# Performance work log

Hardware: AMD Instinct MI355X
Metric: run time of the kernel (lower is better)

## Reference

```python
import jax, jax.numpy as jnp
import numpy as np

N_USERS = 100000
N_ITEMS = 50000
N_NODES = N_USERS + N_ITEMS
EMB_DIM = 64
N_EDGES = 4000000
N_LAYERS = 3
BATCH = 4096


def setup_inputs() -> dict:
    key = jax.random.key(0)
    k = jax.random.split(key, 7)
    return {
        "user_emb": jax.random.normal(k[0], (N_USERS, EMB_DIM), dtype=jnp.float32) * 0.1,
        "item_emb": jax.random.normal(k[1], (N_ITEMS, EMB_DIM), dtype=jnp.float32) * 0.1,
        "vals": jax.random.uniform(k[2], (N_EDGES,), dtype=jnp.float32),
        "src": jax.random.randint(k[3], (N_EDGES,), 0, N_NODES, dtype=jnp.int32),
        "dst": jax.random.randint(k[4], (N_EDGES,), 0, N_NODES, dtype=jnp.int32),
        "users": jax.random.randint(k[5], (BATCH,), 0, N_USERS, dtype=jnp.int32),
        "items": jax.random.randint(k[6], (BATCH,), 0, N_ITEMS, dtype=jnp.int32),
    }


def _propagate(user_emb, item_emb, vals, src, dst):
    # all_emb: [N, D]; sparse adjacency A given as COO (src -> dst, weight vals)
    all_emb = jnp.concatenate([user_emb, item_emb], axis=0)
    acc = all_emb  # running sum over layers (layer 0 included)
    emb = all_emb
    for _ in range(N_LAYERS):
        # SpMM: out[d] = sum_{e: dst[e]==d} vals[e] * emb[src[e]]
        msgs = vals[:, None] * emb[src]               # [E, D]
        emb = jax.ops.segment_sum(msgs, dst, num_segments=N_NODES)
        acc = acc + emb
    light_out = acc / jnp.float32(N_LAYERS + 1)       # mean over stacked layers
    return light_out[:N_USERS], light_out[N_USERS:]


def reference(user_emb, item_emb, vals, src, dst, users, items):
    all_users, all_items = _propagate(user_emb, item_emb, vals, src, dst)
    u = all_users[users]                              # [B, D]
    i = all_items[items]                              # [B, D]
    gamma = jnp.sum(u * i, axis=1)                    # [B]
    return gamma
```

## Files before the change

kernel.cpp:

```cpp
#include <hip/hip_runtime.h>
#include <hip/hip_bf16.h>

#define N_USERS 100000
#define N_ITEMS 50000
#define N_NODES 150000
#define DIM 64
#define N_EDGES 4000000
#define BATCH 4096

#define NBKT 256
#define BW 588
#define STRIDE 16640
#define PA_EDGES 4096
#define PA_ITER 16
#define PA_BLOCKS ((N_EDGES + PA_EDGES - 1) / PA_EDGES)
#define CVT_THREADS (N_NODES * DIM / 8)
#define CVT_BLOCKS 512
#define BS_ITER 32

__device__ __forceinline__ float blo(unsigned int u) { return __uint_as_float(u << 16); }
__device__ __forceinline__ float bhi(unsigned int u) { return __uint_as_float(u & 0xffff0000u); }
__device__ __forceinline__ unsigned int f2b(float f) {
    unsigned int x = __float_as_uint(f);
    return (x + 0x7fffu + ((x >> 16) & 1u)) >> 16;
}
__device__ __forceinline__ unsigned int pack2(float a, float b) {
    return f2b(a) | (f2b(b) << 16);
}

typedef float v2f __attribute__((ext_vector_type(2)));

__global__ void __launch_bounds__(256, 4) k_partition(
        const int* __restrict__ src, const int* __restrict__ dst,
        const float* __restrict__ vals,
        int* __restrict__ gcur, int2* __restrict__ tmp) {
    __shared__ int cnt[NBKT];
    __shared__ int base_s[NBKT];
    __shared__ int off_s[NBKT];
    __shared__ int2 rec_s[PA_EDGES];
    __shared__ unsigned char bin_s[PA_EDGES];
    int t = threadIdx.x;
    int myb[PA_ITER];
    int mykey[PA_ITER];
    int myval[PA_ITER];
    size_t base = (size_t)blockIdx.x * PA_EDGES;
#pragma unroll
    for (int it = 0; it < PA_ITER; it++) {
        size_t i = base + (size_t)it * 256 + t;
        if (i < N_EDGES) {
            myb[it] = __builtin_nontemporal_load(dst + i);
            mykey[it] = __builtin_nontemporal_load(src + i);
            myval[it] = __float_as_int(__builtin_nontemporal_load(vals + i));
        } else {
            myb[it] = -1;
        }
    }
    for (int i = t; i < NBKT; i += 256) cnt[i] = 0;
    __syncthreads();
#pragma unroll
    for (int it = 0; it < PA_ITER; it++) {
        int d = myb[it];
        if (d >= 0) {
            int b = d / BW;
            mykey[it] = (mykey[it] << 10) | (d - b * BW);
            myb[it] = b;
            atomicAdd(&cnt[b], 1);
        }
    }
    __syncthreads();
    {
        int bb = (t + blockIdx.x * 37) & (NBKT - 1);
        int c = cnt[bb];
        base_s[bb] = (c > 0) ? atomicAdd(&gcur[bb], c) : 0;
    }
    if (t < 64) {
        int lane = t;
        int carry = 0;
        for (int c = 0; c < NBKT / 64; c++) {
            int i = c * 64 + lane;
            int x = cnt[i];
            int incl = x;
            for (int o = 1; o < 64; o <<= 1) {
                int y = __shfl_up(incl, o);
                if (lane >= o) incl += y;
            }
            off_s[i] = carry + incl - x;
            carry += __shfl(incl, 63);
        }
    }
    __syncthreads();
    for (int i = t; i < NBKT; i += 256) cnt[i] = 0;
    __syncthreads();
#pragma unroll
    for (int it = 0; it < PA_ITER; it++) {
        int b = myb[it];
        if (b >= 0) {
            int pos = off_s[b] + atomicAdd(&cnt[b], 1);
            rec_s[pos] = make_int2(mykey[it], myval[it]);
            bin_s[pos] = (unsigned char)b;
        }
    }
    __syncthreads();
    int nrec = off_s[NBKT - 1] + cnt[NBKT - 1];
    for (int i = t; i < nrec; i += 256) {
        int2 r = rec_s[i];
        int b = bin_s[i];
        tmp[(size_t)b * STRIDE + base_s[b] + (i - off_s[b])] = r;
    }
}

__global__ void k_bsortcvt(const int2* __restrict__ tmp, const int* __restrict__ gcur,
                           int* __restrict__ row_ptr, int2* __restrict__ fin,
                           const float* __restrict__ uemb, const float* __restrict__ iemb,
                           ushort* __restrict__ ebf0) {
    __shared__ int cnt[BW + 64];
    __shared__ int off[BW + 64];
    __shared__ int gbase_s;
    extern __shared__ int2 rec2[];
    int b = blockIdx.x, t = threadIdx.x;
    if (b >= NBKT) {
        for (int idx = (b - NBKT) * 512 + t; idx < CVT_THREADS; idx += CVT_BLOCKS * 512) {
            int i = idx * 8;
            const float* srcp = (i < N_USERS * DIM) ? (uemb + i) : (iemb + (i - N_USERS * DIM));
            float4 v0, v1;
            v0.x = __builtin_nontemporal_load(srcp + 0);
            v0.y = __builtin_nontemporal_load(srcp + 1);
            v0.z = __builtin_nontemporal_load(srcp + 2);
            v0.w = __builtin_nontemporal_load(srcp + 3);
            v1.x = __builtin_nontemporal_load(srcp + 4);
            v1.y = __builtin_nontemporal_load(srcp + 5);
            v1.z = __builtin_nontemporal_load(srcp + 6);
            v1.w = __builtin_nontemporal_load(srcp + 7);
            uint4 p;
            p.x = pack2(v0.x, v0.y);
            p.y = pack2(v0.z, v0.w);
            p.z = pack2(v1.x, v1.y);
            p.w = pack2(v1.z, v1.w);
            *(uint4*)(ebf0 + i) = p;
        }
        return;
    }
    int node0 = b * BW;
    int nodes = min(BW, N_NODES - node0);
    int count = gcur[b];
    const int2* tb = tmp + (size_t)b * STRIDE;
    int2 myrec[BS_ITER];
#pragma unroll
    for (int it = 0; it < BS_ITER; it++) {
        int e = it * 512 + t;
        myrec[it] = (e < count) ? tb[e] : make_int2(-1, 0);
    }
    if (t < 64) {
        int ssum = 0;
#pragma unroll
        for (int j = 0; j < NBKT / 64; j++) {
            int idx = t * (NBKT / 64) + j;
            if (idx < b) ssum += gcur[idx];
        }
        for (int o = 32; o; o >>= 1) ssum += __shfl_xor(ssum, o);
        if (t == 0) gbase_s = ssum;
    }
    for (int i = t; i < BW + 64; i += 512) cnt[i] = 0;
    __syncthreads();
    int gbase = gbase_s;
#pragma unroll
    for (int it = 0; it < BS_ITER; it++)
        if (myrec[it].x >= 0) atomicAdd(&cnt[myrec[it].x & 1023], 1);
    for (int e = BS_ITER * 512 + t; e < count; e += 512)
        atomicAdd(&cnt[tb[e].x & 1023], 1);
    __syncthreads();
    if (t < 64) {
        int lane = t;
        int carry = 0;
        for (int c = 0; c < 10; c++) {
            int i = c * 64 + lane;
            int x = (i < nodes) ? cnt[i] : 0;
            int incl = x;
            for (int o = 1; o < 64; o <<= 1) {
                int y = __shfl_up(incl, o);
                if (lane >= o) incl += y;
            }
            if (i <= nodes) off[i] = carry + incl - x;
            carry += __shfl(incl, 63);
        }
    }
    __syncthreads();
    for (int i = t; i <= nodes; i += 512)
        if (node0 + i <= N_NODES) row_ptr[node0 + i] = gbase + off[i];
    __syncthreads();
#pragma unroll
    for (int it = 0; it < BS_ITER; it++) {
        int2 r = myrec[it];
        if (r.x >= 0) {
            int pos = atomicAdd(&off[r.x & 1023], 1);
            rec2[pos] = make_int2(r.x >> 10, r.y);
        }
    }
    for (int e = BS_ITER * 512 + t; e < count; e += 512) {
        int2 r = tb[e];
        int pos = atomicAdd(&off[r.x & 1023], 1);
        rec2[pos] = make_int2(r.x >> 10, r.y);
    }
    __syncthreads();
    for (int i = t; i < count; i += 512) fin[gbase + i] = rec2[i];
}


#define EDGE_FMA(r, u, A0, A1, A2, A3)                                        \
    {                                                                         \
        float vf = __int_as_float((r).y);                                     \
        v2f vv = {vf, vf};                                                    \
        v2f f0 = {blo((u).x), bhi((u).x)};                                    \
        v2f f1 = {blo((u).y), bhi((u).y)};                                    \
        v2f f2 = {blo((u).z), bhi((u).z)};                                    \
        v2f f3 = {blo((u).w), bhi((u).w)};                                    \
        A0 = __builtin_elementwise_fma(vv, f0, A0);                           \
        A1 = __builtin_elementwise_fma(vv, f1, A1);                           \
        A2 = __builtin_elementwise_fma(vv, f2, A2);                           \
        A3 = __builtin_elementwise_fma(vv, f3, A3);                           \
    }

#define GATHER16(basec, r) (*(const uint4*)((basec) + ((((unsigned int)(r).x) << 7) | qoff)))
#define REC8(basec, i) (*(const int2*)((basec) + (((unsigned int)(i)) << 3)))

#define BURST32(basec, e, end, last, X0, X1, X2, X3)                          \
    {                                                                         \
        int e1 = (e) + 8, e2 = (e) + 16, e3 = (e) + 24;                       \
        int2 ra = REC8(basec, (e));                                           \
        int2 rb = REC8(basec, min(e1, last));                                 \
        int2 rc = REC8(basec, min(e2, last));                                 \
        int2 rd = REC8(basec, min(e3, last));                                 \
        rb.y = (e1 < (end)) ? rb.y : 0;                                       \
        rc.y = (e2 < (end)) ? rc.y : 0;                                       \
        rd.y = (e3 < (end)) ? rd.y : 0;                                       \
        uint4 ua = GATHER16(einc, ra);                                        \
        uint4 ub = GATHER16(einc, rb);                                        \
        uint4 uc = GATHER16(einc, rc);                                        \
        uint4 ud = GATHER16(einc, rd);                                        \
        EDGE_FMA(ra, ua, X0, X1, X2, X3);                                     \
        EDGE_FMA(rb, ub, X0, X1, X2, X3);                                     \
        EDGE_FMA(rc, uc, X0, X1, X2, X3);                                     \
        EDGE_FMA(rd, ud, X0, X1, X2, X3);                                     \
        (e) += 32;                                                            \
    }

__global__ void k_spmm16(const ushort* __restrict__ ein, ushort* __restrict__ eout,
                         const int* __restrict__ row_ptr, const int2* __restrict__ fin) {
    int wave = (blockIdx.x * blockDim.x + threadIdx.x) >> 6;
    if (wave >= N_NODES) return;
    int lane = threadIdx.x & 63;
    int g = lane >> 3;
    int q = lane & 7;
    unsigned int qoff = (unsigned int)q << 4;
    const char* einc = (const char*)ein;
    const char* finc = (const char*)fin;
    int start = row_ptr[wave], end = row_ptr[wave + 1];
    int last = max(start, end - 1);
    v2f A0 = {0.f, 0.f}, A1 = {0.f, 0.f}, A2 = {0.f, 0.f}, A3 = {0.f, 0.f};
    int e = start + g;
    while (e < end) BURST32(finc, e, end, last, A0, A1, A2, A3);
#pragma unroll
    for (int off = 8; off < 64; off <<= 1) {
        A0.x += __shfl_xor(A0.x, off);
        A0.y += __shfl_xor(A0.y, off);
        A1.x += __shfl_xor(A1.x, off);
        A1.y += __shfl_xor(A1.y, off);
        A2.x += __shfl_xor(A2.x, off);
        A2.y += __shfl_xor(A2.y, off);
        A3.x += __shfl_xor(A3.x, off);
        A3.y += __shfl_xor(A3.y, off);
    }
    if (lane < 8) {
        uint4 p;
        p.x = pack2(A0.x, A0.y);
        p.y = pack2(A1.x, A1.y);
        p.z = pack2(A2.x, A2.y);
        p.w = pack2(A3.x, A3.y);
        *(uint4*)(eout + (size_t)wave * DIM + q * 8) = p;
    }
}

__global__ void k_sampdot(const float* __restrict__ uemb, const float* __restrict__ iemb,
                          const ushort* __restrict__ ebf1, const ushort* __restrict__ ebf2,
                          const int* __restrict__ row_ptr, const int2* __restrict__ fin,
                          const int* __restrict__ users, const int* __restrict__ items,
                          float* __restrict__ out) {
    int b = (blockIdx.x * blockDim.x + threadIdx.x) >> 6;
    if (b >= BATCH) return;
    int lane = threadIdx.x & 63;
    int g = lane >> 3;
    int q = lane & 7;
    unsigned int qoff = (unsigned int)q << 4;
    const char* einc = (const char*)ebf2;
    const char* finc = (const char*)fin;
    int iu = users[b];
    int ii = items[b];
    int nu = iu, ni = ii + N_USERS;
    v2f A0 = {0.f, 0.f}, A1 = {0.f, 0.f}, A2 = {0.f, 0.f}, A3 = {0.f, 0.f};
    {
        int start = row_ptr[nu], end = row_ptr[nu + 1];
        int last = max(start, end - 1);
        int e = start + g;
        while (e < end) BURST32(finc, e, end, last, A0, A1, A2, A3);
    }
    v2f B0 = {0.f, 0.f}, B1 = {0.f, 0.f}, B2 = {0.f, 0.f}, B3 = {0.f, 0.f};
    {
        int start = row_ptr[ni], end = row_ptr[ni + 1];
        int last = max(start, end - 1);
        int e = start + g;
        while (e < end) BURST32(finc, e, end, last, B0, B1, B2, B3);
    }
#pragma unroll
    for (int off = 8; off < 64; off <<= 1) {
        A0.x += __shfl_xor(A0.x, off);
        A0.y += __shfl_xor(A0.y, off);
        A1.x += __shfl_xor(A1.x, off);
        A1.y += __shfl_xor(A1.y, off);
        A2.x += __shfl_xor(A2.x, off);
        A2.y += __shfl_xor(A2.y, off);
        A3.x += __shfl_xor(A3.x, off);
        A3.y += __shfl_xor(A3.y, off);
        B0.x += __shfl_xor(B0.x, off);
        B0.y += __shfl_xor(B0.y, off);
        B1.x += __shfl_xor(B1.x, off);
        B1.y += __shfl_xor(B1.y, off);
        B2.x += __shfl_xor(B2.x, off);
        B2.y += __shfl_xor(B2.y, off);
        B3.x += __shfl_xor(B3.x, off);
        B3.y += __shfl_xor(B3.y, off);
    }
    {
        const float4* fp = (const float4*)(uemb + (size_t)nu * DIM + q * 8);
        float4 fa = fp[0], fb = fp[1];
        uint4 u1 = *(const uint4*)(ebf1 + (size_t)nu * DIM + q * 8);
        uint4 u2 = *(const uint4*)(ebf2 + (size_t)nu * DIM + q * 8);
        A0.x += fa.x + blo(u1.x) + blo(u2.x); A0.y += fa.y + bhi(u1.x) + bhi(u2.x);
        A1.x += fa.z + blo(u1.y) + blo(u2.y); A1.y += fa.w + bhi(u1.y) + bhi(u2.y);
        A2.x += fb.x + blo(u1.z) + blo(u2.z); A2.y += fb.y + bhi(u1.z) + bhi(u2.z);
        A3.x += fb.z + blo(u1.w) + blo(u2.w); A3.y += fb.w + bhi(u1.w) + bhi(u2.w);
    }
    {
        const float4* fp = (const float4*)(iemb + (size_t)ii * DIM + q * 8);
        float4 fa = fp[0], fb = fp[1];
        uint4 u1 = *(const uint4*)(ebf1 + (size_t)ni * DIM + q * 8);
        uint4 u2 = *(const uint4*)(ebf2 + (size_t)ni * DIM + q * 8);
        B0.x += fa.x + blo(u1.x) + blo(u2.x); B0.y += fa.y + bhi(u1.x) + bhi(u2.x);
        B1.x += fa.z + blo(u1.y) + blo(u2.y); B1.y += fa.w + bhi(u1.y) + bhi(u2.y);
        B2.x += fb.x + blo(u1.z) + blo(u2.z); B2.y += fb.y + bhi(u1.z) + bhi(u2.z);
        B3.x += fb.z + blo(u1.w) + blo(u2.w); B3.y += fb.w + bhi(u1.w) + bhi(u2.w);
    }
    float p = A0.x * B0.x + A0.y * B0.y + A1.x * B1.x + A1.y * B1.y +
              A2.x * B2.x + A2.y * B2.y + A3.x * B3.x + A3.y * B3.y;
    p += __shfl_xor(p, 1);
    p += __shfl_xor(p, 2);
    p += __shfl_xor(p, 4);
    if (lane == 0) out[b] = p * (1.0f / 16.0f);
}


extern "C" void kernel_launch(void* const* d_in, const int* in_sizes, int n_in,
                              void* d_out, int out_size, void* d_ws, size_t ws_size,
                              hipStream_t stream) {
    const float* user_emb = (const float*)d_in[0];
    const float* item_emb = (const float*)d_in[1];
    const float* vals = (const float*)d_in[2];
    const int* src = (const int*)d_in[3];
    const int* dst = (const int*)d_in[4];
    const int* users = (const int*)d_in[5];
    const int* items = (const int*)d_in[6];
    float* out = (float*)d_out;

    char* ws = (char*)d_ws;
    size_t off = 0;
    auto alloc = [&](size_t bytes) {
        char* p = ws + off;
        off += (bytes + 255) & ~(size_t)255;
        return p;
    };
    ushort* ebf0 = (ushort*)alloc((size_t)N_NODES * DIM * 2);
    ushort* ebf1 = (ushort*)alloc((size_t)N_NODES * DIM * 2);
    ushort* ebf2 = (ushort*)alloc((size_t)N_NODES * DIM * 2);
    int2* fin = (int2*)alloc((size_t)N_EDGES * 8);
    int* row_ptr = (int*)alloc((size_t)(N_NODES + 1) * 4);
    int* gcur = (int*)alloc((size_t)NBKT * 4);
    int2* tmp = (int2*)ebf1;

    (void)hipMemsetAsync(gcur, 0, (size_t)NBKT * 4, stream);

    k_partition<<<PA_BLOCKS, 256, 0, stream>>>(src, dst, vals, gcur, tmp);
    k_bsortcvt<<<NBKT + CVT_BLOCKS, 512, (size_t)STRIDE * 8, stream>>>(
        tmp, gcur, row_ptr, fin, user_emb, item_emb, ebf0);

    int spmm_blocks = (N_NODES * 64 + 255) / 256;
    k_spmm16<<<spmm_blocks, 256, 0, stream>>>(ebf0, ebf1, row_ptr, fin);
    k_spmm16<<<spmm_blocks, 256, 0, stream>>>(ebf1, ebf2, row_ptr, fin);
    k_sampdot<<<(BATCH * 64 + 255) / 256, 256, 0, stream>>>(
        user_emb, item_emb, ebf1, ebf2, row_ptr, fin, users, items, out);
}
```

Baseline: 311.2 us.

## Skip second-layer SpMM rows not reachable from sampled users and items

The first SpMM launch gains extra blocks that mark, in a bitmap, the sampled user/item nodes and all their in-neighbors. The second SpMM launch then skips rows whose bit is unset, since only those rows feed the final sampled dot products. This cuts gather traffic in the second layer at the cost of a bitmap memset and atomic marking work. Savings depend on what fraction of nodes are reachable, which with dense random graphs may be large.

```diff
diff --git a/kernel.cpp b/kernel.cpp
--- a/kernel.cpp
+++ b/kernel.cpp
@@ -17,6 +17,9 @@
 #define CVT_THREADS (N_NODES * DIM / 8)
 #define CVT_BLOCKS 512
 #define BS_ITER 32
+#define SPMM_BLOCKS ((N_NODES * 64 + 255) / 256)
+#define MARK_BLOCKS 32
+#define BMAP_WORDS ((N_NODES + 31) / 32)
 
 __device__ __forceinline__ float blo(unsigned int u) { return __uint_as_float(u << 16); }
 __device__ __forceinline__ float bhi(unsigned int u) { return __uint_as_float(u & 0xffff0000u); }
@@ -245,9 +248,25 @@
     }
 
 __global__ void k_spmm16(const ushort* __restrict__ ein, ushort* __restrict__ eout,
-                         const int* __restrict__ row_ptr, const int2* __restrict__ fin) {
-    int wave = (blockIdx.x * blockDim.x + threadIdx.x) >> 6;
+                         const int* __restrict__ row_ptr, const int2* __restrict__ fin,
+                         const int* __restrict__ users, const int* __restrict__ items,
+                         unsigned int* __restrict__ bmw, const unsigned int* __restrict__ bmr,
+                         int mark_blocks) {
+    if (blockIdx.x < (unsigned)mark_blocks) {
+        int slot = blockIdx.x * 256 + threadIdx.x;
+        if (slot >= 2 * BATCH) return;
+        int node = (slot < BATCH) ? users[slot] : (items[slot - BATCH] + N_USERS);
+        atomicOr(&bmw[node >> 5], 1u << (node & 31));
+        int s0 = row_ptr[node], s1 = row_ptr[node + 1];
+        for (int e = s0; e < s1; e++) {
+            int s = fin[e].x;
+            atomicOr(&bmw[s >> 5], 1u << (s & 31));
+        }
+        return;
+    }
+    int wave = ((blockIdx.x - mark_blocks) * 256 + (int)threadIdx.x) >> 6;
     if (wave >= N_NODES) return;
+    if (bmr && !((bmr[wave >> 5] >> (wave & 31)) & 1u)) return;
     int lane = threadIdx.x & 63;
     int g = lane >> 3;
     int q = lane & 7;
@@ -383,17 +402,20 @@
     int2* fin = (int2*)alloc((size_t)N_EDGES * 8);
     int* row_ptr = (int*)alloc((size_t)(N_NODES + 1) * 4);
     int* gcur = (int*)alloc((size_t)NBKT * 4);
+    unsigned int* bitmap = (unsigned int*)alloc((size_t)BMAP_WORDS * 4);
     int2* tmp = (int2*)ebf1;
 
     (void)hipMemsetAsync(gcur, 0, (size_t)NBKT * 4, stream);
+    (void)hipMemsetAsync(bitmap, 0, (size_t)BMAP_WORDS * 4, stream);
 
     k_partition<<<PA_BLOCKS, 256, 0, stream>>>(src, dst, vals, gcur, tmp);
     k_bsortcvt<<<NBKT + CVT_BLOCKS, 512, (size_t)STRIDE * 8, stream>>>(
         tmp, gcur, row_ptr, fin, user_emb, item_emb, ebf0);
 
-    int spmm_blocks = (N_NODES * 64 + 255) / 256;
-    k_spmm16<<<spmm_blocks, 256, 0, stream>>>(ebf0, ebf1, row_ptr, fin);
-    k_spmm16<<<spmm_blocks, 256, 0, stream>>>(ebf1, ebf2, row_ptr, fin);
+    k_spmm16<<<MARK_BLOCKS + SPMM_BLOCKS, 256, 0, stream>>>(
+        ebf0, ebf1, row_ptr, fin, users, items, bitmap, nullptr, MARK_BLOCKS);
+    k_spmm16<<<SPMM_BLOCKS, 256, 0, stream>>>(
+        ebf1, ebf2, row_ptr, fin, users, items, nullptr, bitmap, 0);
     k_sampdot<<<(BATCH * 64 + 255) / 256, 256, 0, stream>>>(
         user_emb, item_emb, ebf1, ebf2, row_ptr, fin, users, items, out);
 }
```

Result: no change. 306.3 us (median of 2 runs) (-1.6%).
